# Kernel tuning notes

Measured on AMD Instinct MI355X. Metric: run time of the kernel, lower is better.

Reference implementation:

```python
import jax, jax.numpy as jnp
import numpy as np

DIM = 1024
HEADS = 16
DIM_HEAD = 64
B, N = 2, 2048
EPS_NORM = 1e-12  # F.normalize clamp


def setup_inputs() -> dict:
    key = jax.random.key(0)
    k1, k2, k3 = jax.random.split(key, 3)
    x = jax.random.normal(k1, (B, N, DIM), dtype=jnp.float32)
    gamma = jnp.ones((DIM,), dtype=jnp.float32)
    w_qkv = jax.random.normal(k2, (DIM, 3 * HEADS * DIM_HEAD), dtype=jnp.float32) * (DIM ** -0.5)
    w_out = jax.random.normal(k3, (HEADS * DIM_HEAD, DIM), dtype=jnp.float32) * (DIM ** -0.5)
    return {"x": x, "gamma": gamma, "w_qkv": w_qkv, "w_out": w_out}


def reference(x, gamma, w_qkv, w_out):
    b, n, dim = x.shape
    h, dh = HEADS, DIM_HEAD
    # RMSNorm: F.normalize(x, dim=-1) * sqrt(dim) * gamma
    norm = jnp.maximum(jnp.linalg.norm(x, axis=-1, keepdims=True), EPS_NORM)
    normed = x / norm * (dim ** 0.5) * gamma
    # qkv projection (no bias)
    qkv = normed @ w_qkv  # [b, n, 3*h*dh]
    qkv = qkv.reshape(b, n, 3, h, dh)
    q = qkv[:, :, 0].transpose(0, 2, 1, 3)  # [b, h, n, dh]
    k = qkv[:, :, 1].transpose(0, 2, 1, 3)
    v = qkv[:, :, 2].transpose(0, 2, 1, 3)
    q = q * (dh ** -0.5)
    # attention scores
    sim = jnp.einsum('bhid,bhjd->bhij', q, k)
    mask_value = -jnp.finfo(sim.dtype).max
    # causal mask: triu with offset j - i + 1 (here i == j == n -> offset 1)
    causal_mask = jnp.triu(jnp.ones((n, n), dtype=bool), 1)
    sim = jnp.where(causal_mask, mask_value, sim)
    attn = jax.nn.softmax(sim, axis=-1)
    out = jnp.einsum('bhij,bhjd->bhid', attn, v)
    out = out.transpose(0, 2, 1, 3).reshape(b, n, h * dh)
    return out @ w_out
```

## Files before the change

### kernel.cpp

```cpp
#include <hip/hip_runtime.h>
#include <hip/hip_bf16.h>

typedef unsigned short u16;
using bf16x8 = __attribute__((ext_vector_type(8))) short;
using f32x4  = __attribute__((ext_vector_type(4))) float;
using f32x16 = __attribute__((ext_vector_type(16))) float;
using u32x4  = __attribute__((ext_vector_type(4))) unsigned int;

constexpr int B_ = 2, N_ = 2048, DIM_ = 1024, H_ = 16, DH_ = 64;
constexpr int M_ = B_ * N_;
constexpr int NCQ = 3 * H_ * DH_;

__device__ inline u16 f2bf(float f) {
  union { float f; unsigned u; } v{f};
  unsigned r = v.u + 0x7FFF + ((v.u >> 16) & 1);
  return (u16)(r >> 16);
}

__device__ __forceinline__ void st_pair(u16* p0, u16* p1, float a, float b) {
  unsigned w;
  asm("v_cvt_pk_bf16_f32 %0, %1, %2" : "=v"(w) : "v"(a), "v"(b));
  *p0 = (u16)w;
  *p1 = (u16)(w >> 16);
}

__device__ __forceinline__ void gload16(const u16* g, u16* l) {
  __builtin_amdgcn_global_load_lds(
      (const __attribute__((address_space(1))) unsigned int*)g,
      (__attribute__((address_space(3))) unsigned int*)l, 16, 0, 0);
}

__global__ void __launch_bounds__(256) rmsnorm_kernel(const float* __restrict__ x,
                                                      const float* __restrict__ gamma,
                                                      u16* __restrict__ out) {
  int row = blockIdx.x;
  int t = threadIdx.x;
  const float4 v = reinterpret_cast<const float4*>(x + (size_t)row * DIM_)[t];
  float ss = v.x * v.x + v.y * v.y + v.z * v.z + v.w * v.w;
#pragma unroll
  for (int o = 32; o; o >>= 1) ss += __shfl_down(ss, o, 64);
  __shared__ float partial[4];
  int wid = t >> 6, lane = t & 63;
  if (lane == 0) partial[wid] = ss;
  __syncthreads();
  float tot = partial[0] + partial[1] + partial[2] + partial[3];
  float norm = fmaxf(sqrtf(tot), 1e-12f);
  float scale = 32.0f / norm;
  const float4 g = reinterpret_cast<const float4*>(gamma)[t];
  ushort4 o4;
  o4.x = f2bf(v.x * scale * g.x);
  o4.y = f2bf(v.y * scale * g.y);
  o4.z = f2bf(v.z * scale * g.z);
  o4.w = f2bf(v.w * scale * g.w);
  reinterpret_cast<ushort4*>(out + (size_t)row * DIM_)[t] = o4;
}

__global__ void __launch_bounds__(256) transpose_w_kernel(const float* __restrict__ W,
                                                          u16* __restrict__ WT,
                                                          int K, int Nc) {
  __shared__ float tile[32][33];
  int bc = blockIdx.x * 32;
  int bk = blockIdx.y * 32;
  int tx = threadIdx.x & 31, ty = threadIdx.x >> 5;
#pragma unroll
  for (int r = ty; r < 32; r += 8)
    tile[r][tx] = W[(size_t)(bk + r) * Nc + bc + tx];
  __syncthreads();
#pragma unroll
  for (int r = ty; r < 32; r += 8)
    WT[(size_t)(bc + r) * K + bk + tx] = f2bf(tile[tx][r]);
}

template <int MODE>
__global__ void __launch_bounds__(256) gemm2_kernel(const u16* __restrict__ A,
                                                    const u16* __restrict__ BT,
                                                    void* __restrict__ Cv,
                                                    u16* __restrict__ q_s,
                                                    u16* __restrict__ k_s,
                                                    u16* __restrict__ vt,
                                                    int M, int Nc, int K) {
  __shared__ alignas(16) u16 smem[16384];
  int tid = threadIdx.x;
  int lane = tid & 63, wid = tid >> 6;
  int lr = lane & 15, g = lane >> 4;
  int am0 = (wid >> 1) * 64;
  int bn0 = (wid & 1) * 64;
  int rbase_a = blockIdx.y * 128;
  int rbase_b = blockIdx.x * 128;

  int lineo = tid >> 3;
  int p = tid & 7;
  f32x4 acc[4][4] = {};

#define GSTAGE(base_, src_, rb_, k0_) do {                                           \
    _Pragma("unroll")                                                                \
    for (int c = 0; c < 2; c++) {                                                    \
      int line = c * 32 + lineo;                                                     \
      int sp = p ^ (line & 7);                                                       \
      int row = 2 * line + (sp >> 2);                                                \
      int j = sp & 3;                                                                \
      gload16(src_ + (size_t)(rb_ + row) * K + (k0_) + j * 8,                        \
              (base_) + c * 2048 + wid * 512);                                       \
    }                                                                                \
  } while (0)

#define STAGE(ib_, k0_) do {                                                         \
    GSTAGE(smem + (ib_) * 4096, A, rbase_a, k0_);                                    \
    GSTAGE(smem + 8192 + (ib_) * 4096, BT, rbase_b, k0_);                            \
  } while (0)

  int steps = K >> 5;
  STAGE(0, 0);
  for (int t = 0; t < steps; ++t) {
    int ibuf = t & 1;
    if (t + 1 < steps) {
      STAGE(ibuf ^ 1, (t + 1) * 32);
      asm volatile("s_waitcnt vmcnt(4)" ::: "memory");
    } else {
      asm volatile("s_waitcnt vmcnt(0)" ::: "memory");
    }
    __builtin_amdgcn_s_barrier();
    __builtin_amdgcn_sched_barrier(0);

    const char* ab = (const char*)(smem + ibuf * 4096);
    const char* bb = (const char*)(smem + 8192 + ibuf * 4096);
    bf16x8 a[4], b[4];
#pragma unroll
    for (int mi = 0; mi < 4; mi++) {
      int row = am0 + mi * 16 + lr;
      int byte = (row >> 1) * 128 + ((((row & 1) << 2) + g) ^ ((row >> 1) & 7)) * 16;
      a[mi] = *reinterpret_cast<const bf16x8*>(ab + byte);
    }
#pragma unroll
    for (int ni = 0; ni < 4; ni++) {
      int row = bn0 + ni * 16 + lr;
      int byte = (row >> 1) * 128 + ((((row & 1) << 2) + g) ^ ((row >> 1) & 7)) * 16;
      b[ni] = *reinterpret_cast<const bf16x8*>(bb + byte);
    }
#pragma unroll
    for (int mi = 0; mi < 4; mi++)
#pragma unroll
      for (int ni = 0; ni < 4; ni++)
        acc[mi][ni] = __builtin_amdgcn_mfma_f32_16x16x32_bf16(a[mi], b[ni], acc[mi][ni], 0, 0, 0);

    __builtin_amdgcn_sched_barrier(0);
    __builtin_amdgcn_s_barrier();
  }

  int orow = g * 4;
  if (MODE == 1) {
#pragma unroll
    for (int mi = 0; mi < 4; mi++)
#pragma unroll
      for (int ni = 0; ni < 4; ni++)
#pragma unroll
        for (int r = 0; r < 4; r++) {
          int row = rbase_a + am0 + 16 * mi + orow + r;
          int col = rbase_b + bn0 + 16 * ni + lr;
          ((float*)Cv)[(size_t)row * Nc + col] = acc[mi][ni][r];
        }
  } else {
    int colbase = rbase_b + bn0;
    int region = colbase >> 10;
    int head = (colbase >> 6) & 15;
    const float QS = 0.125f * 1.4426950408889634f;
    if (region < 2) {
#pragma unroll
      for (int mi = 0; mi < 4; mi++)
#pragma unroll
        for (int ni = 0; ni < 4; ni++)
#pragma unroll
          for (int r = 0; r < 4; r += 2) {
            int row = rbase_a + am0 + 16 * mi + orow + r;
            int n = row & 2047, bb_ = row >> 11;
            float v0 = acc[mi][ni][r], v1 = acc[mi][ni][r + 1];
            size_t d0 = ((size_t)(bb_ * 16 + head) * 2048 + n) * 64 + 16 * ni + lr;
            if (region == 0)
              st_pair(q_s + d0, q_s + d0 + 64, v0 * QS, v1 * QS);
            else
              st_pair(k_s + d0, k_s + d0 + 64, v0, v1);
          }
    } else {
      u16* tlds = smem + wid * 4096;
      int n_base = (rbase_a + am0) & 2047;
      int bq = (rbase_a + am0) >> 11;
#pragma unroll
      for (int mi = 0; mi < 4; mi++)
#pragma unroll
        for (int ni = 0; ni < 4; ni++) {
          int n_loc = mi * 16 + orow;
          int dh_loc = ni * 16 + lr;
          unsigned w0, w1;
          asm("v_cvt_pk_bf16_f32 %0, %1, %2"
              : "=v"(w0) : "v"(acc[mi][ni][0]), "v"(acc[mi][ni][1]));
          asm("v_cvt_pk_bf16_f32 %0, %1, %2"
              : "=v"(w1) : "v"(acc[mi][ni][2]), "v"(acc[mi][ni][3]));
          int byte = dh_loc * 128 + ((n_loc * 2) ^ ((dh_loc & 7) << 4));
          uint2 val; val.x = w0; val.y = w1;
          *reinterpret_cast<uint2*>((char*)tlds + byte) = val;
        }
#pragma unroll
      for (int it = 0; it < 8; it++) {
        int dh_loc = it * 8 + (lane >> 3);
        int n8 = (lane & 7) * 8;
        int byte = dh_loc * 128 + ((n8 * 2) ^ ((dh_loc & 7) << 4));
        bf16x8 v = *reinterpret_cast<const bf16x8*>((const char*)tlds + byte);
        size_t dst = ((size_t)(bq * 16 + head) * 64 + dh_loc) * 2048 + n_base + n8;
        *reinterpret_cast<bf16x8*>(vt + dst) = v;
      }
    }
  }
#undef STAGE
#undef GSTAGE
}

__global__ void __launch_bounds__(256) attn6_kernel(const u16* __restrict__ q_s,
                                                    const u16* __restrict__ k_s,
                                                    const u16* __restrict__ vt,
                                                    u16* __restrict__ ao) {
  __shared__ alignas(16) u16 smem[24576];
  int tid = threadIdx.x;
  int lane = tid & 63, wid = tid >> 6;
  int q31 = lane & 31, hi = lane >> 5;
  int strip = wid >> 1, myhalf = wid & 1;
  int blk = blockIdx.x;
  int bh = blk & 31;
  int s = blk >> 5;
  int j = (s & 1) ? (s >> 1) : (31 - (s >> 1));
  int b = bh >> 4, h = bh & 15;
  const u16* qp = q_s + (size_t)bh * N_ * DH_;
  const u16* kp = k_s + (size_t)bh * N_ * DH_;
  const u16* vp = vt + (size_t)bh * DH_ * N_;
  int q0w = j * 64 + strip * 32;
  int qi = q0w + q31;
  int steps = j + 1;

  bf16x8 qf[4];
#pragma unroll
  for (int c = 0; c < 4; c++)
    qf[c] = *reinterpret_cast<const bf16x8*>(qp + (size_t)(q0w + q31) * 64 + c * 16 + hi * 8);

  f32x16 o0 = {}, o1 = {};
  float lsum = 0.f;

  int srow = lane >> 3;
  int scol = (lane & 7) ^ srow;
  int c0 = wid * 2, c1 = c0 + 1;

#define STAGE(rb_, kv0_) do {                                                                \
    gload16(kp + (size_t)((kv0_) + c0 * 8 + srow) * 64 + scol * 8,                           \
            smem + (rb_) * 4096 + c0 * 512);                                                 \
    gload16(kp + (size_t)((kv0_) + c1 * 8 + srow) * 64 + scol * 8,                           \
            smem + (rb_) * 4096 + c1 * 512);                                                 \
    gload16(vp + (size_t)(c0 * 8 + srow) * N_ + (kv0_) + scol * 8,                           \
            smem + 12288 + (rb_) * 4096 + c0 * 512);                                         \
    gload16(vp + (size_t)(c1 * 8 + srow) * N_ + (kv0_) + scol * 8,                           \
            smem + 12288 + (rb_) * 4096 + c1 * 512);                                         \
  } while (0)

  STAGE(0, 0);
  if (steps > 1) STAGE(1, 64);

  int cur = 0, pre = 2;
  for (int t = 0; t < steps; ++t) {
    if (t + 2 < steps) {
      STAGE(pre, (t + 2) * 64);
      pre = (pre == 2) ? 0 : pre + 1;
      asm volatile("s_waitcnt vmcnt(8)" ::: "memory");
    } else if (t + 1 < steps) {
      asm volatile("s_waitcnt vmcnt(4)" ::: "memory");
    } else {
      asm volatile("s_waitcnt vmcnt(0)" ::: "memory");
    }
    __builtin_amdgcn_s_barrier();
    __builtin_amdgcn_sched_barrier(0);

    const u16* kb = smem + cur * 4096;
    const u16* vb = smem + 12288 + cur * 4096;
    cur = (cur == 2) ? 0 : cur + 1;
    int kv = t * 64 + myhalf * 32;
    if (kv <= q0w + 31) {
      f32x16 st = {};
      int krow = myhalf * 32 + q31;
      int ksw = (krow & 7) << 4;
      __builtin_amdgcn_s_setprio(1);
#pragma unroll
      for (int c = 0; c < 4; c++) {
        bf16x8 kf = *reinterpret_cast<const bf16x8*>(
            (const char*)kb + krow * 128 + (((c * 2 + hi) * 16) ^ ksw));
        st = __builtin_amdgcn_mfma_f32_32x32x16_bf16(kf, qf[c], st, 0, 0, 0);
      }
      __builtin_amdgcn_s_setprio(0);
      float p[16];
      bool diag = (kv + 31 > q0w);
      if (diag) {
#pragma unroll
        for (int r = 0; r < 16; r++) {
          int key = kv + (r & 3) + 8 * (r >> 2) + 4 * hi;
          float e = __builtin_amdgcn_exp2f(st[r]);
          p[r] = (key > qi) ? 0.f : e;
        }
      } else {
#pragma unroll
        for (int r = 0; r < 16; r++) p[r] = __builtin_amdgcn_exp2f(st[r]);
      }
#pragma unroll
      for (int r = 0; r < 16; r++) lsum += p[r];
      unsigned cw0[4], cw1[4];
#pragma unroll
      for (int jq = 0; jq < 4; jq++) {
        asm("v_cvt_pk_bf16_f32 %0, %1, %2" : "=v"(cw0[jq]) : "v"(p[4 * jq]), "v"(p[4 * jq + 1]));
        asm("v_cvt_pk_bf16_f32 %0, %1, %2" : "=v"(cw1[jq]) : "v"(p[4 * jq + 2]), "v"(p[4 * jq + 3]));
      }
#pragma unroll
      for (int kc = 0; kc < 2; kc++) {
        unsigned c0a = cw0[2 * kc], c0b = cw0[2 * kc + 1];
        unsigned c1a = cw1[2 * kc], c1b = cw1[2 * kc + 1];
        unsigned sel0 = hi ? c0a : c0b;
        unsigned sel1 = hi ? c1a : c1b;
        unsigned r0 = (unsigned)__shfl_xor((int)sel0, 32, 64);
        unsigned r1 = (unsigned)__shfl_xor((int)sel1, 32, 64);
        u32x4 w;
        w[0] = hi ? r0 : c0a;
        w[1] = hi ? r1 : c1a;
        w[2] = hi ? c0b : r0;
        w[3] = hi ? c1b : r1;
        bf16x8 pa = __builtin_bit_cast(bf16x8, w);
        int slot = (myhalf * 4 + kc * 2 + hi) * 16;
        int vsw = (q31 & 7) << 4;
        bf16x8 vf0 = *reinterpret_cast<const bf16x8*>(
            (const char*)vb + q31 * 128 + (slot ^ vsw));
        bf16x8 vf1 = *reinterpret_cast<const bf16x8*>(
            (const char*)vb + (32 + q31) * 128 + (slot ^ vsw));
        __builtin_amdgcn_s_setprio(1);
        o0 = __builtin_amdgcn_mfma_f32_32x32x16_bf16(pa, vf0, o0, 0, 0, 0);
        o1 = __builtin_amdgcn_mfma_f32_32x32x16_bf16(pa, vf1, o1, 0, 0, 0);
        __builtin_amdgcn_s_setprio(0);
      }
    }
    __builtin_amdgcn_sched_barrier(0);
    __builtin_amdgcn_s_barrier();
  }

  __syncthreads();
  float lc = lsum + __shfl_xor(lsum, 32, 64);
  float* cb = (float*)smem;
  int pr = wid >> 1;
  if (myhalf) {
#pragma unroll
    for (int r = 0; r < 16; r++) {
      cb[pr * 2048 + r * 64 + lane] = o0[r];
      cb[pr * 2048 + (16 + r) * 64 + lane] = o1[r];
    }
    cb[4096 + pr * 64 + lane] = lc;
  }
  __syncthreads();
  if (!myhalf) {
#pragma unroll
    for (int r = 0; r < 16; r++) {
      o0[r] += cb[pr * 2048 + r * 64 + lane];
      o1[r] += cb[pr * 2048 + (16 + r) * 64 + lane];
    }
    float ltot = fmaxf(lc + cb[4096 + pr * 64 + lane], 1e-30f);
    float linv = 1.0f / ltot;
#pragma unroll
    for (int r = 0; r < 16; r += 2) {
      int qrow0 = (r & 3) + 8 * (r >> 2) + 4 * hi;
      float li0 = __shfl(linv, qrow0, 64);
      float li1 = __shfl(linv, qrow0 + 1, 64);
      size_t base0 = (size_t)(b * N_ + q0w + qrow0) * 1024 + h * 64;
      st_pair(ao + base0 + q31, ao + base0 + 1024 + q31, o0[r] * li0, o0[r + 1] * li1);
      st_pair(ao + base0 + 32 + q31, ao + base0 + 1024 + 32 + q31, o1[r] * li0, o1[r + 1] * li1);
    }
  }
#undef STAGE
}

extern "C" void kernel_launch(void* const* d_in, const int* in_sizes, int n_in,
                              void* d_out, int out_size, void* d_ws, size_t ws_size,
                              hipStream_t stream) {
  const float* x = (const float*)d_in[0];
  const float* gamma = (const float*)d_in[1];
  const float* w_qkv = (const float*)d_in[2];
  const float* w_out = (const float*)d_in[3];
  float* out = (float*)d_out;

  char* p = (char*)d_ws;
  u16* normed = (u16*)p; p += (size_t)M_ * DIM_ * 2;
  u16* wt_qkv = (u16*)p; p += (size_t)NCQ * DIM_ * 2;
  u16* wt_out = (u16*)p; p += (size_t)DIM_ * DIM_ * 2;
  u16* k_s = (u16*)p;    p += (size_t)M_ * DIM_ * 2;
  u16* vt = (u16*)p;     p += (size_t)M_ * DIM_ * 2;
  u16* q_s = (u16*)p;    p += (size_t)M_ * DIM_ * 2;
  u16* ao = (u16*)p;     p += (size_t)M_ * DIM_ * 2;

  hipLaunchKernelGGL(rmsnorm_kernel, dim3(M_), dim3(256), 0, stream, x, gamma, normed);
  hipLaunchKernelGGL(transpose_w_kernel, dim3(NCQ / 32, DIM_ / 32), dim3(256), 0, stream,
                     w_qkv, wt_qkv, DIM_, NCQ);
  hipLaunchKernelGGL(transpose_w_kernel, dim3(DIM_ / 32, DIM_ / 32), dim3(256), 0, stream,
                     w_out, wt_out, DIM_, DIM_);
  hipLaunchKernelGGL(gemm2_kernel<2>, dim3(NCQ / 128, M_ / 128), dim3(256), 0, stream,
                     normed, wt_qkv, nullptr, q_s, k_s, vt, M_, NCQ, DIM_);
  hipLaunchKernelGGL(attn6_kernel, dim3(B_ * H_ * (N_ / 64)), dim3(256), 0, stream,
                     q_s, k_s, vt, ao);
  hipLaunchKernelGGL(gemm2_kernel<1>, dim3(DIM_ / 128, M_ / 128), dim3(256), 0, stream,
                     ao, wt_out, (void*)out, nullptr, nullptr, nullptr, M_, DIM_, DIM_);
}
```

Measured before the change: 110.7 us.

## Split attention into 32-query blocks with two waves and double buffering

The attention kernel now gives each block a single 32-query strip handled by two waves that split each 64-key tile, instead of two strips per 256-thread block. The grid doubles and is ordered longest-first, which is meant to improve occupancy and load balance across CUs. LDS staging drops from a triple buffer to a double buffer, reducing shared memory per block but shortening the prefetch distance. Each K/V tile is now loaded once per 32 queries rather than per 64, which doubles K/V global traffic.

```diff
diff --git a/kernel.cpp b/kernel.cpp
--- a/kernel.cpp
+++ b/kernel.cpp
@@ -214,26 +214,24 @@
 #undef GSTAGE
 }
 
-__global__ void __launch_bounds__(256) attn6_kernel(const u16* __restrict__ q_s,
+__global__ void __launch_bounds__(128) attn7_kernel(const u16* __restrict__ q_s,
                                                     const u16* __restrict__ k_s,
                                                     const u16* __restrict__ vt,
                                                     u16* __restrict__ ao) {
-  __shared__ alignas(16) u16 smem[24576];
+  __shared__ alignas(16) u16 smem[16384];
   int tid = threadIdx.x;
-  int lane = tid & 63, wid = tid >> 6;
+  int lane = tid & 63, myhalf = tid >> 6;
   int q31 = lane & 31, hi = lane >> 5;
-  int strip = wid >> 1, myhalf = wid & 1;
   int blk = blockIdx.x;
   int bh = blk & 31;
-  int s = blk >> 5;
-  int j = (s & 1) ? (s >> 1) : (31 - (s >> 1));
+  int jq = 63 - (blk >> 5);
   int b = bh >> 4, h = bh & 15;
   const u16* qp = q_s + (size_t)bh * N_ * DH_;
   const u16* kp = k_s + (size_t)bh * N_ * DH_;
   const u16* vp = vt + (size_t)bh * DH_ * N_;
-  int q0w = j * 64 + strip * 32;
+  int q0w = jq * 32;
   int qi = q0w + q31;
-  int steps = j + 1;
+  int steps = (jq >> 1) + 1;
 
   bf16x8 qf[4];
 #pragma unroll
@@ -245,39 +243,33 @@
 
   int srow = lane >> 3;
   int scol = (lane & 7) ^ srow;
-  int c0 = wid * 2, c1 = c0 + 1;
-
-#define STAGE(rb_, kv0_) do {                                                                \
-    gload16(kp + (size_t)((kv0_) + c0 * 8 + srow) * 64 + scol * 8,                           \
-            smem + (rb_) * 4096 + c0 * 512);                                                 \
-    gload16(kp + (size_t)((kv0_) + c1 * 8 + srow) * 64 + scol * 8,                           \
-            smem + (rb_) * 4096 + c1 * 512);                                                 \
-    gload16(vp + (size_t)(c0 * 8 + srow) * N_ + (kv0_) + scol * 8,                           \
-            smem + 12288 + (rb_) * 4096 + c0 * 512);                                         \
-    gload16(vp + (size_t)(c1 * 8 + srow) * N_ + (kv0_) + scol * 8,                           \
-            smem + 12288 + (rb_) * 4096 + c1 * 512);                                         \
+
+#define STAGE(ib_, kv0_) do {                                                                \
+    _Pragma("unroll")                                                                        \
+    for (int cc = 0; cc < 4; cc++) {                                                         \
+      int c = myhalf * 4 + cc;                                                               \
+      gload16(kp + (size_t)((kv0_) + c * 8 + srow) * 64 + scol * 8,                          \
+              smem + (ib_) * 4096 + c * 512);                                                \
+      gload16(vp + (size_t)(c * 8 + srow) * N_ + (kv0_) + scol * 8,                          \
+              smem + 8192 + (ib_) * 4096 + c * 512);                                         \
+    }                                                                                        \
   } while (0)
 
   STAGE(0, 0);
-  if (steps > 1) STAGE(1, 64);
-
-  int cur = 0, pre = 2;
+
   for (int t = 0; t < steps; ++t) {
-    if (t + 2 < steps) {
-      STAGE(pre, (t + 2) * 64);
-      pre = (pre == 2) ? 0 : pre + 1;
+    int ibuf = t & 1;
+    if (t + 1 < steps) {
+      STAGE(ibuf ^ 1, (t + 1) * 64);
       asm volatile("s_waitcnt vmcnt(8)" ::: "memory");
-    } else if (t + 1 < steps) {
-      asm volatile("s_waitcnt vmcnt(4)" ::: "memory");
     } else {
       asm volatile("s_waitcnt vmcnt(0)" ::: "memory");
     }
     __builtin_amdgcn_s_barrier();
     __builtin_amdgcn_sched_barrier(0);
 
-    const u16* kb = smem + cur * 4096;
-    const u16* vb = smem + 12288 + cur * 4096;
-    cur = (cur == 2) ? 0 : cur + 1;
+    const u16* kb = smem + ibuf * 4096;
+    const u16* vb = smem + 8192 + ibuf * 4096;
     int kv = t * 64 + myhalf * 32;
     if (kv <= q0w + 31) {
       f32x16 st = {};
@@ -308,9 +300,9 @@
       for (int r = 0; r < 16; r++) lsum += p[r];
       unsigned cw0[4], cw1[4];
 #pragma unroll
-      for (int jq = 0; jq < 4; jq++) {
-        asm("v_cvt_pk_bf16_f32 %0, %1, %2" : "=v"(cw0[jq]) : "v"(p[4 * jq]), "v"(p[4 * jq + 1]));
-        asm("v_cvt_pk_bf16_f32 %0, %1, %2" : "=v"(cw1[jq]) : "v"(p[4 * jq + 2]), "v"(p[4 * jq + 3]));
+      for (int jj = 0; jj < 4; jj++) {
+        asm("v_cvt_pk_bf16_f32 %0, %1, %2" : "=v"(cw0[jj]) : "v"(p[4 * jj]), "v"(p[4 * jj + 1]));
+        asm("v_cvt_pk_bf16_f32 %0, %1, %2" : "=v"(cw1[jj]) : "v"(p[4 * jj + 2]), "v"(p[4 * jj + 3]));
       }
 #pragma unroll
       for (int kc = 0; kc < 2; kc++) {
@@ -345,23 +337,22 @@
   __syncthreads();
   float lc = lsum + __shfl_xor(lsum, 32, 64);
   float* cb = (float*)smem;
-  int pr = wid >> 1;
   if (myhalf) {
 #pragma unroll
     for (int r = 0; r < 16; r++) {
-      cb[pr * 2048 + r * 64 + lane] = o0[r];
-      cb[pr * 2048 + (16 + r) * 64 + lane] = o1[r];
-    }
-    cb[4096 + pr * 64 + lane] = lc;
+      cb[r * 64 + lane] = o0[r];
+      cb[(16 + r) * 64 + lane] = o1[r];
+    }
+    cb[2048 + lane] = lc;
   }
   __syncthreads();
   if (!myhalf) {
 #pragma unroll
     for (int r = 0; r < 16; r++) {
-      o0[r] += cb[pr * 2048 + r * 64 + lane];
-      o1[r] += cb[pr * 2048 + (16 + r) * 64 + lane];
-    }
-    float ltot = fmaxf(lc + cb[4096 + pr * 64 + lane], 1e-30f);
+      o0[r] += cb[r * 64 + lane];
+      o1[r] += cb[(16 + r) * 64 + lane];
+    }
+    float ltot = fmaxf(lc + cb[2048 + lane], 1e-30f);
     float linv = 1.0f / ltot;
 #pragma unroll
     for (int r = 0; r < 16; r += 2) {
@@ -401,7 +392,7 @@
                      w_out, wt_out, DIM_, DIM_);
   hipLaunchKernelGGL(gemm2_kernel<2>, dim3(NCQ / 128, M_ / 128), dim3(256), 0, stream,
                      normed, wt_qkv, nullptr, q_s, k_s, vt, M_, NCQ, DIM_);
-  hipLaunchKernelGGL(attn6_kernel, dim3(B_ * H_ * (N_ / 64)), dim3(256), 0, stream,
+  hipLaunchKernelGGL(attn7_kernel, dim3(B_ * H_ * (N_ / 32)), dim3(128), 0, stream,
                      q_s, k_s, vt, ao);
   hipLaunchKernelGGL(gemm2_kernel<1>, dim3(DIM_ / 128, M_ / 128), dim3(256), 0, stream,
                      ao, wt_out, (void*)out, nullptr, nullptr, nullptr, M_, DIM_, DIM_);
```

After: 116.5 us. 1.05x slower.
